# Kernel optimization log

Hardware: AMD Instinct MI355X
Metric: run time of the kernel (lower is better)

The kernel has to match this reference:

```python
import jax, jax.numpy as jnp
import numpy as np
import jax.lax as lax
from jax.scipy.special import logsumexp

N, T, C = 512, 1024, 64  # batch, seq len, n_classes


def setup_inputs() -> dict:
    key = jax.random.key(0)
    k1, k2, k3, k4 = jax.random.split(key, 4)
    batch_logits = jax.random.normal(k1, (N, T, C), dtype=jnp.float32)
    # learned CRF transition matrix; (i,j) = score of transitioning j -> i
    transition_matrix = jax.random.normal(k2, (C, C), dtype=jnp.float32) * 0.1
    init_alphas = jnp.zeros((C,), dtype=jnp.float32)
    lengths = jax.random.randint(k3, (N,), 2, T + 1)
    batch_tags = jax.random.randint(k4, (N, T), 0, C)
    return dict(batch_logits=batch_logits, transition_matrix=transition_matrix,
                init_alphas=init_alphas, lengths=lengths, batch_tags=batch_tags)


def _log_partition_scores(trans, init_alphas, logits):
    """sum_scores: logZ of all sequences of length (i+2), shape [T-1]."""
    def step(prev_alphas, logit_t):
        # core_recursion with fn=logsumexp: [C,1] + [C,C] + [1,C] -> lse over axis 1
        new = logsumexp(logit_t[:, None] + trans + prev_alphas[None, :], axis=1)
        return new, logsumexp(new, axis=-1)
    _, scores = lax.scan(step, init_alphas + logits[0], logits[1:])
    return scores


def _gold_scores(trans, init_alphas, logits, tags):
    """score_sequence: score of gold prefix of length (i+2), shape [T-1]."""
    first = init_alphas[tags[0]] + logits[0, tags[0]]
    # step increments: transition[tags[t+1], tags[t]] + logits[t+1, tags[t+1]]
    steps = trans[tags[1:], tags[:-1]] + \
        jnp.take_along_axis(logits[1:], tags[1:, None], axis=1)[:, 0]
    return first + jnp.cumsum(steps)


def reference(batch_logits, transition_matrix, init_alphas, lengths, batch_tags):
    # CRF negative log-likelihood per sequence: logZ(length) - gold_score(length)
    logZ_all = jax.vmap(lambda lg: _log_partition_scores(transition_matrix, init_alphas, lg))(batch_logits)
    gold_all = jax.vmap(lambda lg, tg: _gold_scores(transition_matrix, init_alphas, lg, tg))(batch_logits, batch_tags)
    idx = (lengths - 2)[:, None]  # pick the entry at the true sequence length
    logZ = jnp.take_along_axis(logZ_all, idx, axis=1)[:, 0]
    gold = jnp.take_along_axis(gold_all, idx, axis=1)[:, 0]
    return logZ - gold  # [N]
```

## Files before the change

### kernel.cpp

```cpp
#include <hip/hip_runtime.h>
#include <cstdint>
#include <cstddef>

#define NC 64
#define LN2 0.6931471805599453f

typedef _Float16 half2_t __attribute__((ext_vector_type(2)));
typedef unsigned int uint32x4 __attribute__((ext_vector_type(4)));

static __device__ __forceinline__ float dot2acc(uint32_t a, uint32_t b, float c) {
#if __has_builtin(__builtin_amdgcn_fdot2)
    return __builtin_amdgcn_fdot2(__builtin_bit_cast(half2_t, a),
                                  __builtin_bit_cast(half2_t, b), c, false);
#else
    half2_t ha = __builtin_bit_cast(half2_t, a), hb = __builtin_bit_cast(half2_t, b);
    return c + (float)ha[0] * (float)hb[0] + (float)ha[1] * (float)hb[1];
#endif
}

template <int CTRL>
static __device__ __forceinline__ float dppf(float x) {
    return __int_as_float(__builtin_amdgcn_update_dpp(
        0, __float_as_int(x), CTRL, 0xf, 0xf, true));
}
static __device__ __forceinline__ float wave_sum_bcast(float x) {
    x = x + dppf<0x111>(x);
    x = x + dppf<0x112>(x);
    x = x + dppf<0x114>(x);
    x = x + dppf<0x118>(x);
    x = x + dppf<0x142>(x);
    x = x + dppf<0x143>(x);
    return __int_as_float(__builtin_amdgcn_readlane(__float_as_int(x), 63));
}

__global__ __launch_bounds__(128, 1)
void crf_nll_kernel(const float* __restrict__ logits,
                    const float* __restrict__ trans,
                    const float* __restrict__ init_alphas,
                    const int*  __restrict__ lengths,
                    const int*  __restrict__ tags,
                    float* __restrict__ out,
                    int N, int T)
{
    const int n = blockIdx.x;
    const int tid = threadIdx.x;
    const int wid = tid >> 6;
    const int lane = tid & 63;
    const float* lg = logits + (size_t)n * T * NC;
    const int len = lengths[n];
    const int Tm1 = T - 1;

    __shared__ __align__(16) uint32_t Etab[2][64 * 32];
    __shared__ __align__(16) uint16_t st_pk[2][NC + 8];
    __shared__ __align__(16) float xchg[2][NC];
    __shared__ float Lsh[2], gsh[2];

    #pragma unroll
    for (int i = tid; i < 2 * 64 * 32; i += 128) {
        int tab = i >> 11, idx = i & 2047;
        int row = idx >> 5, k = idx & 31;
        float x0 = (tab == 0) ? trans[row * NC + 2 * k]     : trans[(2 * k) * NC + row];
        float x1 = (tab == 0) ? trans[row * NC + 2 * k + 1] : trans[(2 * k + 1) * NC + row];
        uint32_t lo = (uint32_t)__builtin_bit_cast(uint16_t, (_Float16)__expf(x0));
        uint32_t hi = (uint32_t)__builtin_bit_cast(uint16_t, (_Float16)__expf(x1));
        Etab[tab][idx] = lo | (hi << 16);
    }
    __syncthreads();

    uint32x4 e0, e1, e2, e3, e4, e5, e6, e7;
    {
        uint32_t e_addr = (uint32_t)(uintptr_t)&Etab[wid][0] + (uint32_t)(lane * 128);
        asm volatile(
            "ds_read_b128 %0, %8 offset:0\n\t"
            "ds_read_b128 %1, %8 offset:16\n\t"
            "ds_read_b128 %2, %8 offset:32\n\t"
            "ds_read_b128 %3, %8 offset:48\n\t"
            "ds_read_b128 %4, %8 offset:64\n\t"
            "ds_read_b128 %5, %8 offset:80\n\t"
            "ds_read_b128 %6, %8 offset:96\n\t"
            "ds_read_b128 %7, %8 offset:112\n\t"
            "s_waitcnt lgkmcnt(0)"
            : "=&v"(e0), "=&v"(e1), "=&v"(e2), "=&v"(e3),
              "=&v"(e4), "=&v"(e5), "=&v"(e6), "=&v"(e7)
            : "v"(e_addr)
            : "memory");
        __builtin_amdgcn_sched_barrier(0);
    }

    const int m  = (len - 1) >> 1;
    const int nb = len - 1 - m;

    const uint32x4* vb4 = reinterpret_cast<const uint32x4*>(st_pk[wid]);
    uint16_t* my_pk = st_pk[wid];

    float L = 0.f, vcur = 1.0f, s_cur = 1.0f, dL = 0.0f;

    auto dotE = [&]() -> float {
        float c0 = 0.f, c1 = 0.f, c2 = 0.f, c3 = 0.f;
        float c4 = 0.f, c5 = 0.f, c6 = 0.f, c7 = 0.f;
        uint32x4 w;
        w = vb4[0];
        c0 = dot2acc(e0.x, w.x, c0); c1 = dot2acc(e0.y, w.y, c1);
        c2 = dot2acc(e0.z, w.z, c2); c3 = dot2acc(e0.w, w.w, c3);
        w = vb4[1];
        c4 = dot2acc(e1.x, w.x, c4); c5 = dot2acc(e1.y, w.y, c5);
        c6 = dot2acc(e1.z, w.z, c6); c7 = dot2acc(e1.w, w.w, c7);
        w = vb4[2];
        c0 = dot2acc(e2.x, w.x, c0); c1 = dot2acc(e2.y, w.y, c1);
        c2 = dot2acc(e2.z, w.z, c2); c3 = dot2acc(e2.w, w.w, c3);
        w = vb4[3];
        c4 = dot2acc(e3.x, w.x, c4); c5 = dot2acc(e3.y, w.y, c5);
        c6 = dot2acc(e3.z, w.z, c6); c7 = dot2acc(e3.w, w.w, c7);
        w = vb4[4];
        c0 = dot2acc(e4.x, w.x, c0); c1 = dot2acc(e4.y, w.y, c1);
        c2 = dot2acc(e4.z, w.z, c2); c3 = dot2acc(e4.w, w.w, c3);
        w = vb4[5];
        c4 = dot2acc(e5.x, w.x, c4); c5 = dot2acc(e5.y, w.y, c5);
        c6 = dot2acc(e5.z, w.z, c6); c7 = dot2acc(e5.w, w.w, c7);
        w = vb4[6];
        c0 = dot2acc(e6.x, w.x, c0); c1 = dot2acc(e6.y, w.y, c1);
        c2 = dot2acc(e6.z, w.z, c2); c3 = dot2acc(e6.w, w.w, c3);
        w = vb4[7];
        c4 = dot2acc(e7.x, w.x, c4); c5 = dot2acc(e7.y, w.y, c5);
        c6 = dot2acc(e7.z, w.z, c6); c7 = dot2acc(e7.w, w.w, c7);
        return ((c0 + c4) + (c1 + c5)) + ((c2 + c6) + (c3 + c7));
    };

    if (wid == 0) {
        float a0 = init_alphas[lane] + lg[lane];
        L = __int_as_float(__builtin_amdgcn_readfirstlane(__float_as_int(a0))) + 8.f * LN2;
        vcur = __expf(a0 - L);
        my_pk[lane] = __builtin_bit_cast(uint16_t, (_Float16)vcur);

        auto fstep = [&](float raw) {
            float fs = __expf(raw) * s_cur;
            L += dL;
            float v = fs * dotE();
            vcur = v;
            my_pk[lane] = __builtin_bit_cast(uint16_t, (_Float16)v);
            unsigned bits = (unsigned)__builtin_amdgcn_readfirstlane((int)__float_as_uint(v));
            int e = (int)((bits >> 23) & 0xFF);
            s_cur = __uint_as_float((unsigned)(246 - e) << 23);
            dL    = (float)(e - 119) * LN2;
        };

        float r0 = lg[NC * (1 < Tm1 ? 1 : Tm1) + lane];
        float r1 = lg[NC * (2 < Tm1 ? 2 : Tm1) + lane];
        float r2 = lg[NC * (3 < Tm1 ? 3 : Tm1) + lane];
        float r3 = lg[NC * (4 < Tm1 ? 4 : Tm1) + lane];
        float r4 = lg[NC * (5 < Tm1 ? 5 : Tm1) + lane];
        float r5 = lg[NC * (6 < Tm1 ? 6 : Tm1) + lane];
        float r6 = lg[NC * (7 < Tm1 ? 7 : Tm1) + lane];
        float r7 = lg[NC * (8 < Tm1 ? 8 : Tm1) + lane];

        int t = 1;
        for (; t + 8 <= m + 1; t += 8) {
            int p;
            fstep(r0); p = t +  8; p = p < Tm1 ? p : Tm1; r0 = lg[NC * p + lane];
            fstep(r1); p = t +  9; p = p < Tm1 ? p : Tm1; r1 = lg[NC * p + lane];
            fstep(r2); p = t + 10; p = p < Tm1 ? p : Tm1; r2 = lg[NC * p + lane];
            fstep(r3); p = t + 11; p = p < Tm1 ? p : Tm1; r3 = lg[NC * p + lane];
            fstep(r4); p = t + 12; p = p < Tm1 ? p : Tm1; r4 = lg[NC * p + lane];
            fstep(r5); p = t + 13; p = p < Tm1 ? p : Tm1; r5 = lg[NC * p + lane];
            fstep(r6); p = t + 14; p = p < Tm1 ? p : Tm1; r6 = lg[NC * p + lane];
            fstep(r7); p = t + 15; p = p < Tm1 ? p : Tm1; r7 = lg[NC * p + lane];
        }
        if (t + 0 <= m) fstep(r0);
        if (t + 1 <= m) fstep(r1);
        if (t + 2 <= m) fstep(r2);
        if (t + 3 <= m) fstep(r3);
        if (t + 4 <= m) fstep(r4);
        if (t + 5 <= m) fstep(r5);
        if (t + 6 <= m) fstep(r6);
    } else {
        auto bstep = [&](float raw) {
            float p = __expf(raw) * s_cur * vcur;
            L += dL;
            my_pk[lane] = __builtin_bit_cast(uint16_t, (_Float16)p);
            float u = dotE();
            vcur = u;
            unsigned bits = (unsigned)__builtin_amdgcn_readfirstlane((int)__float_as_uint(u));
            int e = (int)((bits >> 23) & 0xFF);
            s_cur = __uint_as_float((unsigned)(246 - e) << 23);
            dL    = (float)(e - 119) * LN2;
        };

        int p0;
        p0 = len - 1;     p0 = p0 > 1 ? p0 : 1; float r0 = lg[NC * p0 + lane];
        p0 = len - 2;     p0 = p0 > 1 ? p0 : 1; float r1 = lg[NC * p0 + lane];
        p0 = len - 3;     p0 = p0 > 1 ? p0 : 1; float r2 = lg[NC * p0 + lane];
        p0 = len - 4;     p0 = p0 > 1 ? p0 : 1; float r3 = lg[NC * p0 + lane];
        p0 = len - 5;     p0 = p0 > 1 ? p0 : 1; float r4 = lg[NC * p0 + lane];
        p0 = len - 6;     p0 = p0 > 1 ? p0 : 1; float r5 = lg[NC * p0 + lane];
        p0 = len - 7;     p0 = p0 > 1 ? p0 : 1; float r6 = lg[NC * p0 + lane];
        p0 = len - 8;     p0 = p0 > 1 ? p0 : 1; float r7 = lg[NC * p0 + lane];

        int k = 0;
        for (; k + 8 <= nb; k += 8) {
            int p;
            bstep(r0); p = len - 1 - (k +  8); p = p > 1 ? p : 1; r0 = lg[NC * p + lane];
            bstep(r1); p = len - 1 - (k +  9); p = p > 1 ? p : 1; r1 = lg[NC * p + lane];
            bstep(r2); p = len - 1 - (k + 10); p = p > 1 ? p : 1; r2 = lg[NC * p + lane];
            bstep(r3); p = len - 1 - (k + 11); p = p > 1 ? p : 1; r3 = lg[NC * p + lane];
            bstep(r4); p = len - 1 - (k + 12); p = p > 1 ? p : 1; r4 = lg[NC * p + lane];
            bstep(r5); p = len - 1 - (k + 13); p = p > 1 ? p : 1; r5 = lg[NC * p + lane];
            bstep(r6); p = len - 1 - (k + 14); p = p > 1 ? p : 1; r6 = lg[NC * p + lane];
            bstep(r7); p = len - 1 - (k + 15); p = p > 1 ? p : 1; r7 = lg[NC * p + lane];
        }
        if (k + 0 < nb) bstep(r0);
        if (k + 1 < nb) bstep(r1);
        if (k + 2 < nb) bstep(r2);
        if (k + 3 < nb) bstep(r3);
        if (k + 4 < nb) bstep(r4);
        if (k + 5 < nb) bstep(r5);
        if (k + 6 < nb) bstep(r6);
    }

    xchg[wid][lane] = vcur;
    if (lane == 0) Lsh[wid] = L;

    const int* tg = tags + (size_t)n * T;
    float g = 0.f;
    for (int tt = 1 + tid; tt < len; tt += 128) {
        const int cur = tg[tt];
        const int prv = tg[tt - 1];
        g += trans[cur * NC + prv] + lg[tt * NC + cur];
    }
    g = wave_sum_bcast(g);
    if (lane == 0) gsh[wid] = g;

    __syncthreads();

    if (wid == 0) {
        float prod = xchg[0][lane] * xchg[1][lane];
        float ssum = wave_sum_bcast(prod);
        if (lane == 0) {
            float logZ = Lsh[0] + Lsh[1] + __logf(ssum);
            int t0v = tg[0];
            float gold = init_alphas[t0v] + lg[t0v] + gsh[0] + gsh[1];
            out[n] = logZ - gold;
        }
    }
}

extern "C" void kernel_launch(void* const* d_in, const int* in_sizes, int n_in,
                              void* d_out, int out_size, void* d_ws, size_t ws_size,
                              hipStream_t stream)
{
    const float* logits = (const float*)d_in[0];
    const float* trans  = (const float*)d_in[1];
    const float* inita  = (const float*)d_in[2];
    const int*   lens   = (const int*)d_in[3];
    const int*   tags   = (const int*)d_in[4];
    float*       out    = (float*)d_out;

    const int N = 512, T = 1024;
    crf_nll_kernel<<<N, 128, 0, stream>>>(logits, trans, inita, lens, tags, out, N, T);
}
```

Baseline: 136.4 us.

## Swizzle exp-transition table so each lane reads one vector chunk, reduce via DPP

Reorders the fp16 exp(transition) table so each lane holds entries for eight rows that are XOR-swizzled against one 8-element chunk of the state vector. Each lane then does a single 16-byte LDS read per step instead of eight broadcast reads, computes eight partial dot products, and combines them across neighbouring lanes with DPP quad-permute and row-shift operations. The goal is less LDS traffic and shorter latency on the serial recurrence step. In exchange it adds cross-lane DPP dependencies and relies on the swizzle being exactly correct.

Result: faster. 131.4 us (median of 2 runs) (-3.7%).

```diff
diff --git a/kernel.cpp b/kernel.cpp
--- a/kernel.cpp
+++ b/kernel.cpp
@@ -32,6 +32,7 @@
     x = x + dppf<0x143>(x);
     return __int_as_float(__builtin_amdgcn_readlane(__float_as_int(x), 63));
 }
+
 
 __global__ __launch_bounds__(128, 1)
 void crf_nll_kernel(const float* __restrict__ logits,
@@ -56,14 +57,19 @@
     __shared__ float Lsh[2], gsh[2];
 
     #pragma unroll
-    for (int i = tid; i < 2 * 64 * 32; i += 128) {
-        int tab = i >> 11, idx = i & 2047;
-        int row = idx >> 5, k = idx & 31;
-        float x0 = (tab == 0) ? trans[row * NC + 2 * k]     : trans[(2 * k) * NC + row];
-        float x1 = (tab == 0) ? trans[row * NC + 2 * k + 1] : trans[(2 * k + 1) * NC + row];
+    for (int idx = tid; idx < 2 * 64 * 32; idx += 128) {
+        int tab = idx >> 11, rem = idx & 2047;
+        int i = rem >> 5, wrd = rem & 31;
+        int j = wrd >> 2, k = wrd & 3;
+        int D = (j & 3) | ((j & 4) << 1);
+        int row = i ^ D;
+        int s = (i & 3) | ((i >> 1) & 4);
+        int c0 = 8 * s + 2 * k, c1 = c0 + 1;
+        float x0 = tab == 0 ? trans[row * NC + c0] : trans[c0 * NC + row];
+        float x1 = tab == 0 ? trans[row * NC + c1] : trans[c1 * NC + row];
         uint32_t lo = (uint32_t)__builtin_bit_cast(uint16_t, (_Float16)__expf(x0));
         uint32_t hi = (uint32_t)__builtin_bit_cast(uint16_t, (_Float16)__expf(x1));
-        Etab[tab][idx] = lo | (hi << 16);
+        Etab[tab][i * 32 + wrd] = lo | (hi << 16);
     }
     __syncthreads();
 
@@ -90,40 +96,31 @@
     const int m  = (len - 1) >> 1;
     const int nb = len - 1 - m;
 
-    const uint32x4* vb4 = reinterpret_cast<const uint32x4*>(st_pk[wid]);
     uint16_t* my_pk = st_pk[wid];
+    const int s_lane = (lane & 3) | ((lane >> 1) & 4);
+    const uint32x4* wchunk = reinterpret_cast<const uint32x4*>(my_pk + 8 * s_lane);
 
     float L = 0.f, vcur = 1.0f, s_cur = 1.0f, dL = 0.0f;
 
     auto dotE = [&]() -> float {
-        float c0 = 0.f, c1 = 0.f, c2 = 0.f, c3 = 0.f;
-        float c4 = 0.f, c5 = 0.f, c6 = 0.f, c7 = 0.f;
-        uint32x4 w;
-        w = vb4[0];
-        c0 = dot2acc(e0.x, w.x, c0); c1 = dot2acc(e0.y, w.y, c1);
-        c2 = dot2acc(e0.z, w.z, c2); c3 = dot2acc(e0.w, w.w, c3);
-        w = vb4[1];
-        c4 = dot2acc(e1.x, w.x, c4); c5 = dot2acc(e1.y, w.y, c5);
-        c6 = dot2acc(e1.z, w.z, c6); c7 = dot2acc(e1.w, w.w, c7);
-        w = vb4[2];
-        c0 = dot2acc(e2.x, w.x, c0); c1 = dot2acc(e2.y, w.y, c1);
-        c2 = dot2acc(e2.z, w.z, c2); c3 = dot2acc(e2.w, w.w, c3);
-        w = vb4[3];
-        c4 = dot2acc(e3.x, w.x, c4); c5 = dot2acc(e3.y, w.y, c5);
-        c6 = dot2acc(e3.z, w.z, c6); c7 = dot2acc(e3.w, w.w, c7);
-        w = vb4[4];
-        c0 = dot2acc(e4.x, w.x, c0); c1 = dot2acc(e4.y, w.y, c1);
-        c2 = dot2acc(e4.z, w.z, c2); c3 = dot2acc(e4.w, w.w, c3);
-        w = vb4[5];
-        c4 = dot2acc(e5.x, w.x, c4); c5 = dot2acc(e5.y, w.y, c5);
-        c6 = dot2acc(e5.z, w.z, c6); c7 = dot2acc(e5.w, w.w, c7);
-        w = vb4[6];
-        c0 = dot2acc(e6.x, w.x, c0); c1 = dot2acc(e6.y, w.y, c1);
-        c2 = dot2acc(e6.z, w.z, c2); c3 = dot2acc(e6.w, w.w, c3);
-        w = vb4[7];
-        c4 = dot2acc(e7.x, w.x, c4); c5 = dot2acc(e7.y, w.y, c5);
-        c6 = dot2acc(e7.z, w.z, c6); c7 = dot2acc(e7.w, w.w, c7);
-        return ((c0 + c4) + (c1 + c5)) + ((c2 + c6) + (c3 + c7));
+        const uint32x4 w = wchunk[0];
+        float p0, p1, p2, p3, p4, p5, p6, p7;
+        p0 = dot2acc(e0.x, w.x, dot2acc(e0.y, w.y, dot2acc(e0.z, w.z, dot2acc(e0.w, w.w, 0.f))));
+        p1 = dot2acc(e1.x, w.x, dot2acc(e1.y, w.y, dot2acc(e1.z, w.z, dot2acc(e1.w, w.w, 0.f))));
+        p2 = dot2acc(e2.x, w.x, dot2acc(e2.y, w.y, dot2acc(e2.z, w.z, dot2acc(e2.w, w.w, 0.f))));
+        p3 = dot2acc(e3.x, w.x, dot2acc(e3.y, w.y, dot2acc(e3.z, w.z, dot2acc(e3.w, w.w, 0.f))));
+        p4 = dot2acc(e4.x, w.x, dot2acc(e4.y, w.y, dot2acc(e4.z, w.z, dot2acc(e4.w, w.w, 0.f))));
+        p5 = dot2acc(e5.x, w.x, dot2acc(e5.y, w.y, dot2acc(e5.z, w.z, dot2acc(e5.w, w.w, 0.f))));
+        p6 = dot2acc(e6.x, w.x, dot2acc(e6.y, w.y, dot2acc(e6.z, w.z, dot2acc(e6.w, w.w, 0.f))));
+        p7 = dot2acc(e7.x, w.x, dot2acc(e7.y, w.y, dot2acc(e7.z, w.z, dot2acc(e7.w, w.w, 0.f))));
+        float q0  = p0 + dppf<0xB1>(p1);
+        float q2  = p2 + dppf<0xB1>(p3);
+        float q8  = p4 + dppf<0xB1>(p5);
+        float q10 = p6 + dppf<0xB1>(p7);
+        float r0 = q0 + dppf<0x4E>(q2);
+        float r8 = q8 + dppf<0x4E>(q10);
+        float t8 = dppf<0x141>(r8);
+        return r0 + dppf<0x140>(t8);
     };
 
     if (wid == 0) {
@@ -185,15 +182,15 @@
             dL    = (float)(e - 119) * LN2;
         };
 
-        int p0;
-        p0 = len - 1;     p0 = p0 > 1 ? p0 : 1; float r0 = lg[NC * p0 + lane];
-        p0 = len - 2;     p0 = p0 > 1 ? p0 : 1; float r1 = lg[NC * p0 + lane];
-        p0 = len - 3;     p0 = p0 > 1 ? p0 : 1; float r2 = lg[NC * p0 + lane];
-        p0 = len - 4;     p0 = p0 > 1 ? p0 : 1; float r3 = lg[NC * p0 + lane];
-        p0 = len - 5;     p0 = p0 > 1 ? p0 : 1; float r4 = lg[NC * p0 + lane];
-        p0 = len - 6;     p0 = p0 > 1 ? p0 : 1; float r5 = lg[NC * p0 + lane];
-        p0 = len - 7;     p0 = p0 > 1 ? p0 : 1; float r6 = lg[NC * p0 + lane];
-        p0 = len - 8;     p0 = p0 > 1 ? p0 : 1; float r7 = lg[NC * p0 + lane];
+        int p0i;
+        p0i = len - 1; p0i = p0i > 1 ? p0i : 1; float r0 = lg[NC * p0i + lane];
+        p0i = len - 2; p0i = p0i > 1 ? p0i : 1; float r1 = lg[NC * p0i + lane];
+        p0i = len - 3; p0i = p0i > 1 ? p0i : 1; float r2 = lg[NC * p0i + lane];
+        p0i = len - 4; p0i = p0i > 1 ? p0i : 1; float r3 = lg[NC * p0i + lane];
+        p0i = len - 5; p0i = p0i > 1 ? p0i : 1; float r4 = lg[NC * p0i + lane];
+        p0i = len - 6; p0i = p0i > 1 ? p0i : 1; float r5 = lg[NC * p0i + lane];
+        p0i = len - 7; p0i = p0i > 1 ? p0i : 1; float r6 = lg[NC * p0i + lane];
+        p0i = len - 8; p0i = p0i > 1 ? p0i : 1; float r7 = lg[NC * p0i + lane];
 
         int k = 0;
         for (; k + 8 <= nb; k += 8) {
```
